# Kernel optimization log

Measured on AMD Instinct MI355X. Metric: run time of the kernel, lower is better.

## Reference

```python
import jax, jax.numpy as jnp
import numpy as np

BIG = 1e9  # finite stand-in for float('inf') border padding (grad-safe)


def setup_inputs() -> dict:
    key = jax.random.key(0)
    k1, k2 = jax.random.split(key)
    B, L1, L2, F = 32, 1024, 1024, 128
    return {
        "seq1": jax.random.normal(k1, (B, L1, F), dtype=jnp.float32),
        "seq2": jax.random.normal(k2, (B, L2, F), dtype=jnp.float32),
        "scale_weights": jnp.ones((1,), dtype=jnp.float32),  # nn.Parameter ones(num_scales)/num_scales -> softmax-normalized anyway
    }


def _dtw_similarity(seq1, seq2):
    """Vectorized (anti-diagonal wavefront) version of MultiScaleDTW._compute_dtw.

    Same recurrence: D[i,j] = ||s1[i-1]-s2[j-1]|| + min(D[i-1,j-1], D[i-1,j], D[i,j-1]),
    D[0,0]=0, first row/col = inf. Returns similarity = 1/(1 + D[L1,L2]/(L1+L2)).
    """
    B, L1, F = seq1.shape
    L2 = seq2.shape[1]
    # pairwise L2 distance matrix (B, L1, L2) via |a|^2 + |b|^2 - 2 a.b (one GEMM)
    sq1 = jnp.sum(seq1 * seq1, axis=-1)
    sq2 = jnp.sum(seq2 * seq2, axis=-1)
    dot = jnp.einsum('bif,bjf->bij', seq1, seq2)
    C = jnp.sqrt(jnp.maximum(sq1[:, :, None] + sq2[:, None, :] - 2.0 * dot, 0.0))

    i_idx = jnp.arange(L1 + 1)
    # diagonal k holds D[i, k-i] for i in [0, L1]
    d0 = jnp.full((B, L1 + 1), BIG, jnp.float32).at[:, 0].set(0.0)  # k=0: D[0,0]=0
    d1 = jnp.full((B, L1 + 1), BIG, jnp.float32)                     # k=1: borders = inf

    def shift(x):  # x[:, i] -> x[:, i-1], pad with BIG
        return jnp.concatenate([jnp.full((B, 1), BIG, x.dtype), x[:, :-1]], axis=1)

    def step(carry, k):
        prev2, prev = carry  # diagonals k-2, k-1
        j = k - i_idx
        row = jnp.clip(i_idx - 1, 0, L1 - 1)
        col = jnp.clip(j - 1, 0, L2 - 1)
        c = C[:, row, col]  # (B, L1+1) cost along the diagonal
        m = jnp.minimum(shift(prev2), jnp.minimum(shift(prev), prev))
        cur = c + m
        valid = (i_idx >= 1) & (i_idx <= L1) & (j >= 1) & (j <= L2)
        cur = jnp.where(valid[None, :], cur, BIG)
        return (prev, cur), None

    (_, last), _ = jax.lax.scan(step, (d0, d1), jnp.arange(2, L1 + L2 + 1))
    dtw_dist = last[:, L1] / (L1 + L2)  # D[L1, L2] / (L1 + L2)
    return 1.0 / (1.0 + dtw_dist)


def reference(seq1, seq2, scale_weights):
    # num_scales = 1: softmax over single scale weight -> 1.0; only scale-0 DTW runs
    w = jax.nn.softmax(scale_weights, axis=0)
    sim = _dtw_similarity(seq1, seq2)
    return w[0] * sim  # combined_similarity, shape (B,)
```

## Files before the change

kernel.cpp:

```cpp
#include <hip/hip_runtime.h>
#include <hip/hip_bf16.h>

#define BIGV 1.0e9f

static constexpr int B_ = 32;
static constexpr int L_ = 1024;
static constexpr int F_ = 128;
static constexpr int S_ = 2;
static constexpr int UDIM_ = 1296;
static constexpr int LAG_ = 160;
static constexpr int NSEGG_ = 82;
static constexpr size_t STREAM_US = (size_t)B_ * 2 * UDIM_ * 512;

typedef __attribute__((ext_vector_type(8))) short short8;
typedef __attribute__((ext_vector_type(4))) float f32x4;

__device__ __forceinline__ unsigned pack2(float x, float y) {
  unsigned r;
  asm("v_cvt_pk_bf16_f32 %0, %1, %2" : "=v"(r) : "v"(x), "v"(y));
  return r;
}

__global__ void norm_kernel(const float* __restrict__ s1, const float* __restrict__ s2,
                            float* __restrict__ nrm) {
  int gt   = blockIdx.x * blockDim.x + threadIdx.x;
  int wid  = gt >> 6;
  int lane = gt & 63;
  const float* src = (wid < B_ * L_) ? (s1 + (size_t)wid * F_)
                                     : (s2 + (size_t)(wid - B_ * L_) * F_);
  float2 v = ((const float2*)src)[lane];
  float s = v.x * v.x + v.y * v.y;
#pragma unroll
  for (int o = 32; o > 0; o >>= 1) s += __shfl_xor(s, o, 64);
  if (lane == 0) nrm[wid] = s;
}

__global__ __launch_bounds__(256) void cost_kernel(const float* __restrict__ s1,
                                                   const float* __restrict__ s2,
                                                   ushort* __restrict__ stream,
                                                   const float* __restrict__ nrm) {
  __shared__ __align__(16) ushort sbuf[2 * 128 * 136];
  __shared__ float q1[128], q2[128];
  short (*aL)[136] = (short(*)[136])sbuf;
  short (*bL)[136] = (short(*)[136])(sbuf + 128 * 136);
  ushort (*stage)[136] = (ushort(*)[136])sbuf;

  const int tid = threadIdx.x;
  const int b   = blockIdx.y;
  const int tc  = blockIdx.x & 7;
  const int tr  = blockIdx.x >> 3;

  const float* Ap = s1 + (size_t)b * L_ * F_ + (size_t)tr * 128 * F_;
  const float* Bp = s2 + (size_t)b * L_ * F_ + (size_t)tc * 128 * F_;

#pragma unroll 4
  for (int it = 0; it < 16; ++it) {
    int idx = it * 1024 + tid * 4;
    int r = idx >> 7, cc = idx & 127;
    float4 va = *(const float4*)(Ap + idx);
    float4 vb = *(const float4*)(Bp + idx);
    *(uint2*)&aL[r][cc] = make_uint2(pack2(va.x, va.y), pack2(va.z, va.w));
    *(uint2*)&bL[r][cc] = make_uint2(pack2(vb.x, vb.y), pack2(vb.z, vb.w));
  }
  if (tid < 128) q1[tid] = nrm[(size_t)b * L_ + tr * 128 + tid];
  else           q2[tid - 128] = nrm[(size_t)B_ * L_ + (size_t)b * L_ + tc * 128 + (tid - 128)];
  __syncthreads();

  const int wave = tid >> 6, lane = tid & 63, quad = lane >> 4, l16 = lane & 15;
  const int m0 = (wave >> 1) * 64, n0 = (wave & 1) * 64;

  f32x4 acc[4][4] = {};
#pragma unroll
  for (int kc = 0; kc < 4; ++kc) {
    short8 af[4], bf[4];
#pragma unroll
    for (int mi = 0; mi < 4; ++mi)
      af[mi] = *(const short8*)&aL[m0 + mi * 16 + l16][kc * 32 + quad * 8];
#pragma unroll
    for (int nj = 0; nj < 4; ++nj)
      bf[nj] = *(const short8*)&bL[n0 + nj * 16 + l16][kc * 32 + quad * 8];
#pragma unroll
    for (int mi = 0; mi < 4; ++mi)
#pragma unroll
      for (int nj = 0; nj < 4; ++nj)
        acc[mi][nj] = __builtin_amdgcn_mfma_f32_16x16x32_bf16(af[mi], bf[nj], acc[mi][nj], 0, 0, 0);
  }

  __syncthreads();

#pragma unroll
  for (int mi = 0; mi < 4; ++mi) {
    int lr = m0 + mi * 16 + quad * 4;
    int du = 2 * (lr >> 3);
    float a0 = q1[lr + 0], a1 = q1[lr + 1], a2 = q1[lr + 2], a3 = q1[lr + 3];
#pragma unroll
    for (int nj = 0; nj < 4; ++nj) {
      int lc = n0 + nj * 16 + l16;
      float qc = q2[lc];
      float vx = sqrtf(fmaxf(a0 + qc - 2.0f * acc[mi][nj][0], 0.0f));
      float vy = sqrtf(fmaxf(a1 + qc - 2.0f * acc[mi][nj][1], 0.0f));
      float vz = sqrtf(fmaxf(a2 + qc - 2.0f * acc[mi][nj][2], 0.0f));
      float vw = sqrtf(fmaxf(a3 + qc - 2.0f * acc[mi][nj][3], 0.0f));
      *(uint2*)&stage[lc + du][lr] = make_uint2(pack2(vx, vy), pack2(vz, vw));
    }
  }
  __syncthreads();

  const int w      = tr >> 2;
  const int rlbase = (tr & 3) * 128;
  const int ubase  = tc * 128 + 32 * (tr & 3);
  ushort* Sb = stream + ((size_t)(b * 2 + w) * UDIM_ + ubase) * 512 + rlbase;
#pragma unroll
  for (int it = 0; it < 10; ++it) {
    int t = it * 256 + tid;
    if (t < 158 * 16) {
      int u = t >> 4, g = t & 15;
      if ((unsigned)(u - 2 * g) < 128u)
        *(uint4*)(Sb + (size_t)u * 512 + g * 8) = *(const uint4*)&stage[u][g * 8];
    }
  }
}

#define UNPACK_CV(cw, cv)                         \
  cv[0] = __uint_as_float((cw).x << 16);          \
  cv[1] = __uint_as_float((cw).x & 0xFFFF0000u);  \
  cv[2] = __uint_as_float((cw).y << 16);          \
  cv[3] = __uint_as_float((cw).y & 0xFFFF0000u);  \
  cv[4] = __uint_as_float((cw).z << 16);          \
  cv[5] = __uint_as_float((cw).z & 0xFFFF0000u);  \
  cv[6] = __uint_as_float((cw).w << 16);          \
  cv[7] = __uint_as_float((cw).w & 0xFFFF0000u);

#define CHAIN_BODY(head)                                            \
  {                                                                 \
    float cur = (head);                                             \
    float nl[8];                                                    \
    nl[0] = cur;                                                    \
    _Pragma("unroll") for (int r = 1; r < 8; ++r) {                 \
      cur = cv[r] + fminf(fminf(left[r - 1], left[r]), cur);        \
      nl[r] = cur;                                                  \
    }                                                               \
    _Pragma("unroll") for (int r = 0; r < 8; ++r) left[r] = nl[r];  \
    bot = nl[7];                                                    \
  }

__global__ __launch_bounds__(128, 1) void dtw_kernel(const ushort* __restrict__ stream,
                                                     float* __restrict__ out) {
  __shared__ float hand[1040];

  const int b    = blockIdx.x;
  const int tid  = threadIdx.x;
  const int wave = tid >> 6;
  const int lane = tid & 63;
  const bool l0 = (lane == 0);

  const ushort* src = stream + (size_t)(b * 2 + wave) * UDIM_ * 512 + lane * 8;

  float left[8];
#pragma unroll
  for (int r = 0; r < 8; ++r) left[r] = BIGV;
  float bot = BIGV;
  float sh[4] = {BIGV, BIGV, BIGV, BIGV};
  float hPrev = BIGV, result = 0.0f;
  float hRing[4];
  float hb[16];
  uint4 pre[16];

#pragma unroll
  for (int i = 0; i < 16; ++i) pre[i] = *(const uint4*)(src + (size_t)i * 512);

  for (int n = 0; n < NSEGG_; ++n) {
    __syncthreads();
    const int sBase = 16 * n - (wave ? LAG_ : 0);
    if ((unsigned)sBase >= 1152u) continue;

    const bool fast = (sBase >= 128) & (sBase <= 1008);

    if (wave == 0) {
      if (fast) {
#pragma unroll
        for (int k = 0; k < 16; ++k) {
          float shN = __shfl_up(bot, 1, 64);
          uint4 cw = pre[k];
          pre[k] = *(const uint4*)(src + (size_t)(sBase + k + 16) * 512);
          float cv[8];
          UNPACK_CV(cw, cv)
          float dgT = l0 ? BIGV : sh[(k + 2) & 3];
          float upT = l0 ? BIGV : sh[(k + 3) & 3];
          CHAIN_BODY(cv[0] + fminf(fminf(dgT, upT), left[0]))
          sh[k & 3] = shN;
          hb[k] = bot;
        }
        if (lane == 63) {
          float4* hp = (float4*)&hand[sBase - 126];
          hp[0] = make_float4(hb[0], hb[1], hb[2], hb[3]);
          hp[1] = make_float4(hb[4], hb[5], hb[6], hb[7]);
          hp[2] = make_float4(hb[8], hb[9], hb[10], hb[11]);
          hp[3] = make_float4(hb[12], hb[13], hb[14], hb[15]);
        }
      } else {
#pragma unroll
        for (int k = 0; k < 16; ++k) {
          const int s = sBase + k;
          const int col = s - S_ * lane;
          float shN = __shfl_up(bot, 1, 64);
          uint4 cw = pre[k];
          pre[k] = *(const uint4*)(src + (size_t)(sBase + k + 16) * 512);
          float cv[8];
          UNPACK_CV(cw, cv)
          float dgT = l0 ? ((s == 0) ? 0.0f : BIGV) : sh[(k + 2) & 3];
          float upT = l0 ? BIGV : sh[(k + 3) & 3];
          bool act = ((unsigned)col < 1024u);
          float c0 = act ? cv[0] : BIGV;
          CHAIN_BODY(c0 + fminf(fminf(dgT, upT), left[0]))
          sh[k & 3] = shN;
          int j = s - 126;
          if (lane == 63 && (unsigned)j < 1024u) hand[j] = bot;
        }
      }
    } else {
      if (fast) {
#pragma unroll
        for (int i = 0; i < 4; ++i) hRing[i] = hand[sBase + i];
#pragma unroll
        for (int k = 0; k < 16; ++k) {
          float shN = __shfl_up(bot, 1, 64);
          float hCur = hRing[k & 3];
          uint4 cw = pre[k];
          pre[k] = *(const uint4*)(src + (size_t)(sBase + k + 16) * 512);
          hRing[k & 3] = hand[sBase + k + 4];
          float cv[8];
          UNPACK_CV(cw, cv)
          float dgT = l0 ? hPrev : sh[(k + 2) & 3];
          float upT = l0 ? hCur : sh[(k + 3) & 3];
          CHAIN_BODY(cv[0] + fminf(fminf(dgT, upT), left[0]))
          sh[k & 3] = shN;
          hPrev = hCur;
        }
      } else {
#pragma unroll
        for (int i = 0; i < 4; ++i) hRing[i] = hand[(sBase + i) & 1023];
#pragma unroll
        for (int k = 0; k < 16; ++k) {
          const int s = sBase + k;
          const int col = s - S_ * lane;
          float shN = __shfl_up(bot, 1, 64);
          float hCur = hRing[k & 3];
          uint4 cw = pre[k];
          pre[k] = *(const uint4*)(src + (size_t)(sBase + k + 16) * 512);
          hRing[k & 3] = hand[(s + 4) & 1023];
          float cv[8];
          UNPACK_CV(cw, cv)
          float dgT = l0 ? ((s == 0) ? BIGV : hPrev) : sh[(k + 2) & 3];
          float upT = l0 ? hCur : sh[(k + 3) & 3];
          bool act = ((unsigned)col < 1024u);
          float c0 = act ? cv[0] : BIGV;
          CHAIN_BODY(c0 + fminf(fminf(dgT, upT), left[0]))
          sh[k & 3] = shN;
          hPrev = hCur;
          if (s == 1149) result = bot;
        }
      }
    }
  }
  if (wave == 1 && lane == 63) out[b] = 1.0f / (1.0f + result * (1.0f / 2048.0f));
}

extern "C" void kernel_launch(void* const* d_in, const int* in_sizes, int n_in,
                              void* d_out, int out_size, void* d_ws, size_t ws_size,
                              hipStream_t stream_) {
  const float* s1 = (const float*)d_in[0];
  const float* s2 = (const float*)d_in[1];
  float* out = (float*)d_out;
  ushort* cws = (ushort*)d_ws;
  float* nrm = (float*)(cws + STREAM_US);

  norm_kernel<<<dim3((2 * B_ * L_) / 4), 256, 0, stream_>>>(s1, s2, nrm);
  cost_kernel<<<dim3(64, B_), 256, 0, stream_>>>(s1, s2, cws, nrm);
  dtw_kernel<<<dim3(B_), 128, 0, stream_>>>(cws, out);
}
```

Measured before the change: 237.6 us.

## Split DTW wavefront across four waves with four rows per lane

Each batch's DTW recurrence now runs on four pipelined waves instead of two, each lane handling four rows rather than eight. This shortens the serial dependency chain per diagonal step. The cost-stream layout is repacked to 256-row slices per wave, and boundary rows are handed between consecutive waves through per-wave LDS buffers. In exchange there are more lagged segments, more block barriers and more per-step shuffle overhead relative to the arithmetic.

Result: slower. 256.6 us (+8.0%).

```diff
diff --git a/kernel.cpp b/kernel.cpp
--- a/kernel.cpp
+++ b/kernel.cpp
@@ -9,8 +9,8 @@
 static constexpr int S_ = 2;
 static constexpr int UDIM_ = 1296;
 static constexpr int LAG_ = 160;
-static constexpr int NSEGG_ = 82;
-static constexpr size_t STREAM_US = (size_t)B_ * 2 * UDIM_ * 512;
+static constexpr int NSEGG_ = 102;
+static constexpr size_t STREAM_US = (size_t)B_ * 4 * UDIM_ * 256;
 
 typedef __attribute__((ext_vector_type(8))) short short8;
 typedef __attribute__((ext_vector_type(4))) float f32x4;
@@ -91,7 +91,7 @@
 #pragma unroll
   for (int mi = 0; mi < 4; ++mi) {
     int lr = m0 + mi * 16 + quad * 4;
-    int du = 2 * (lr >> 3);
+    int du = 2 * (lr >> 2);
     float a0 = q1[lr + 0], a1 = q1[lr + 1], a2 = q1[lr + 2], a3 = q1[lr + 3];
 #pragma unroll
     for (int nj = 0; nj < 4; ++nj) {
@@ -106,93 +106,89 @@
   }
   __syncthreads();
 
-  const int w      = tr >> 2;
-  const int rlbase = (tr & 3) * 128;
-  const int ubase  = tc * 128 + 32 * (tr & 3);
-  ushort* Sb = stream + ((size_t)(b * 2 + w) * UDIM_ + ubase) * 512 + rlbase;
-#pragma unroll
-  for (int it = 0; it < 10; ++it) {
+  const int w      = tr >> 1;
+  const int rlbase = (tr & 1) * 128;
+  const int ubase  = tc * 128 + 64 * (tr & 1);
+  ushort* Sb = stream + ((size_t)(b * 4 + w) * UDIM_ + ubase) * 256 + rlbase;
+#pragma unroll
+  for (int it = 0; it < 24; ++it) {
     int t = it * 256 + tid;
-    if (t < 158 * 16) {
-      int u = t >> 4, g = t & 15;
+    if (t < 190 * 32) {
+      int u = t >> 5, g = t & 31;
       if ((unsigned)(u - 2 * g) < 128u)
-        *(uint4*)(Sb + (size_t)u * 512 + g * 8) = *(const uint4*)&stage[u][g * 8];
+        *(uint2*)(Sb + (size_t)u * 256 + g * 4) = *(const uint2*)&stage[u][g * 4];
     }
   }
 }
 
-#define UNPACK_CV(cw, cv)                         \
+#define UNPACK_CV4(cw, cv)                        \
   cv[0] = __uint_as_float((cw).x << 16);          \
   cv[1] = __uint_as_float((cw).x & 0xFFFF0000u);  \
   cv[2] = __uint_as_float((cw).y << 16);          \
-  cv[3] = __uint_as_float((cw).y & 0xFFFF0000u);  \
-  cv[4] = __uint_as_float((cw).z << 16);          \
-  cv[5] = __uint_as_float((cw).z & 0xFFFF0000u);  \
-  cv[6] = __uint_as_float((cw).w << 16);          \
-  cv[7] = __uint_as_float((cw).w & 0xFFFF0000u);
-
-#define CHAIN_BODY(head)                                            \
+  cv[3] = __uint_as_float((cw).y & 0xFFFF0000u);
+
+#define CHAIN_BODY4(head)                                           \
   {                                                                 \
     float cur = (head);                                             \
-    float nl[8];                                                    \
+    float nl[4];                                                    \
     nl[0] = cur;                                                    \
-    _Pragma("unroll") for (int r = 1; r < 8; ++r) {                 \
+    _Pragma("unroll") for (int r = 1; r < 4; ++r) {                 \
       cur = cv[r] + fminf(fminf(left[r - 1], left[r]), cur);        \
       nl[r] = cur;                                                  \
     }                                                               \
-    _Pragma("unroll") for (int r = 0; r < 8; ++r) left[r] = nl[r];  \
-    bot = nl[7];                                                    \
-  }
-
-__global__ __launch_bounds__(128, 1) void dtw_kernel(const ushort* __restrict__ stream,
+    _Pragma("unroll") for (int r = 0; r < 4; ++r) left[r] = nl[r];  \
+    bot = nl[3];                                                    \
+  }
+
+__global__ __launch_bounds__(256, 1) void dtw_kernel(const ushort* __restrict__ stream,
                                                      float* __restrict__ out) {
-  __shared__ float hand[1040];
+  __shared__ float hand[3][1040];
 
   const int b    = blockIdx.x;
   const int tid  = threadIdx.x;
-  const int wave = tid >> 6;
+  const int w    = tid >> 6;
   const int lane = tid & 63;
   const bool l0 = (lane == 0);
 
-  const ushort* src = stream + (size_t)(b * 2 + wave) * UDIM_ * 512 + lane * 8;
-
-  float left[8];
-#pragma unroll
-  for (int r = 0; r < 8; ++r) left[r] = BIGV;
+  const ushort* src = stream + (size_t)(b * 4 + w) * UDIM_ * 256 + lane * 4;
+
+  float left[4];
+#pragma unroll
+  for (int r = 0; r < 4; ++r) left[r] = BIGV;
   float bot = BIGV;
   float sh[4] = {BIGV, BIGV, BIGV, BIGV};
   float hPrev = BIGV, result = 0.0f;
   float hRing[4];
   float hb[16];
-  uint4 pre[16];
-
-#pragma unroll
-  for (int i = 0; i < 16; ++i) pre[i] = *(const uint4*)(src + (size_t)i * 512);
+  uint2 pre[16];
+
+#pragma unroll
+  for (int i = 0; i < 16; ++i) pre[i] = *(const uint2*)(src + (size_t)i * 256);
 
   for (int n = 0; n < NSEGG_; ++n) {
     __syncthreads();
-    const int sBase = 16 * n - (wave ? LAG_ : 0);
+    const int sBase = 16 * n - w * LAG_;
     if ((unsigned)sBase >= 1152u) continue;
 
     const bool fast = (sBase >= 128) & (sBase <= 1008);
 
-    if (wave == 0) {
+    if (w == 0) {
       if (fast) {
 #pragma unroll
         for (int k = 0; k < 16; ++k) {
           float shN = __shfl_up(bot, 1, 64);
-          uint4 cw = pre[k];
-          pre[k] = *(const uint4*)(src + (size_t)(sBase + k + 16) * 512);
-          float cv[8];
-          UNPACK_CV(cw, cv)
+          uint2 cw = pre[k];
+          pre[k] = *(const uint2*)(src + (size_t)(sBase + k + 16) * 256);
+          float cv[4];
+          UNPACK_CV4(cw, cv)
           float dgT = l0 ? BIGV : sh[(k + 2) & 3];
           float upT = l0 ? BIGV : sh[(k + 3) & 3];
-          CHAIN_BODY(cv[0] + fminf(fminf(dgT, upT), left[0]))
+          CHAIN_BODY4(cv[0] + fminf(fminf(dgT, upT), left[0]))
           sh[k & 3] = shN;
           hb[k] = bot;
         }
         if (lane == 63) {
-          float4* hp = (float4*)&hand[sBase - 126];
+          float4* hp = (float4*)&hand[0][sBase - 126];
           hp[0] = make_float4(hb[0], hb[1], hb[2], hb[3]);
           hp[1] = make_float4(hb[4], hb[5], hb[6], hb[7]);
           hp[2] = make_float4(hb[8], hb[9], hb[10], hb[11]);
@@ -204,66 +200,121 @@
           const int s = sBase + k;
           const int col = s - S_ * lane;
           float shN = __shfl_up(bot, 1, 64);
-          uint4 cw = pre[k];
-          pre[k] = *(const uint4*)(src + (size_t)(sBase + k + 16) * 512);
-          float cv[8];
-          UNPACK_CV(cw, cv)
+          uint2 cw = pre[k];
+          pre[k] = *(const uint2*)(src + (size_t)(sBase + k + 16) * 256);
+          float cv[4];
+          UNPACK_CV4(cw, cv)
           float dgT = l0 ? ((s == 0) ? 0.0f : BIGV) : sh[(k + 2) & 3];
           float upT = l0 ? BIGV : sh[(k + 3) & 3];
           bool act = ((unsigned)col < 1024u);
           float c0 = act ? cv[0] : BIGV;
-          CHAIN_BODY(c0 + fminf(fminf(dgT, upT), left[0]))
+          CHAIN_BODY4(c0 + fminf(fminf(dgT, upT), left[0]))
           sh[k & 3] = shN;
           int j = s - 126;
-          if (lane == 63 && (unsigned)j < 1024u) hand[j] = bot;
+          if (lane == 63 && (unsigned)j < 1024u) hand[0][j] = bot;
         }
       }
-    } else {
+    } else if (w == 3) {
+      const float* hs = hand[2];
       if (fast) {
 #pragma unroll
-        for (int i = 0; i < 4; ++i) hRing[i] = hand[sBase + i];
+        for (int i = 0; i < 4; ++i) hRing[i] = hs[sBase + i];
 #pragma unroll
         for (int k = 0; k < 16; ++k) {
           float shN = __shfl_up(bot, 1, 64);
           float hCur = hRing[k & 3];
-          uint4 cw = pre[k];
-          pre[k] = *(const uint4*)(src + (size_t)(sBase + k + 16) * 512);
-          hRing[k & 3] = hand[sBase + k + 4];
-          float cv[8];
-          UNPACK_CV(cw, cv)
+          uint2 cw = pre[k];
+          pre[k] = *(const uint2*)(src + (size_t)(sBase + k + 16) * 256);
+          hRing[k & 3] = hs[sBase + k + 4];
+          float cv[4];
+          UNPACK_CV4(cw, cv)
           float dgT = l0 ? hPrev : sh[(k + 2) & 3];
           float upT = l0 ? hCur : sh[(k + 3) & 3];
-          CHAIN_BODY(cv[0] + fminf(fminf(dgT, upT), left[0]))
+          CHAIN_BODY4(cv[0] + fminf(fminf(dgT, upT), left[0]))
           sh[k & 3] = shN;
           hPrev = hCur;
         }
       } else {
 #pragma unroll
-        for (int i = 0; i < 4; ++i) hRing[i] = hand[(sBase + i) & 1023];
+        for (int i = 0; i < 4; ++i) hRing[i] = hs[(sBase + i) & 1023];
 #pragma unroll
         for (int k = 0; k < 16; ++k) {
           const int s = sBase + k;
           const int col = s - S_ * lane;
           float shN = __shfl_up(bot, 1, 64);
           float hCur = hRing[k & 3];
-          uint4 cw = pre[k];
-          pre[k] = *(const uint4*)(src + (size_t)(sBase + k + 16) * 512);
-          hRing[k & 3] = hand[(s + 4) & 1023];
-          float cv[8];
-          UNPACK_CV(cw, cv)
+          uint2 cw = pre[k];
+          pre[k] = *(const uint2*)(src + (size_t)(sBase + k + 16) * 256);
+          hRing[k & 3] = hs[(s + 4) & 1023];
+          float cv[4];
+          UNPACK_CV4(cw, cv)
           float dgT = l0 ? ((s == 0) ? BIGV : hPrev) : sh[(k + 2) & 3];
           float upT = l0 ? hCur : sh[(k + 3) & 3];
           bool act = ((unsigned)col < 1024u);
           float c0 = act ? cv[0] : BIGV;
-          CHAIN_BODY(c0 + fminf(fminf(dgT, upT), left[0]))
+          CHAIN_BODY4(c0 + fminf(fminf(dgT, upT), left[0]))
           sh[k & 3] = shN;
           hPrev = hCur;
           if (s == 1149) result = bot;
         }
       }
+    } else {
+      const float* hs = hand[w - 1];
+      float* hd = hand[w];
+      if (fast) {
+#pragma unroll
+        for (int i = 0; i < 4; ++i) hRing[i] = hs[sBase + i];
+#pragma unroll
+        for (int k = 0; k < 16; ++k) {
+          float shN = __shfl_up(bot, 1, 64);
+          float hCur = hRing[k & 3];
+          uint2 cw = pre[k];
+          pre[k] = *(const uint2*)(src + (size_t)(sBase + k + 16) * 256);
+          hRing[k & 3] = hs[sBase + k + 4];
+          float cv[4];
+          UNPACK_CV4(cw, cv)
+          float dgT = l0 ? hPrev : sh[(k + 2) & 3];
+          float upT = l0 ? hCur : sh[(k + 3) & 3];
+          CHAIN_BODY4(cv[0] + fminf(fminf(dgT, upT), left[0]))
+          sh[k & 3] = shN;
+          hPrev = hCur;
+          hb[k] = bot;
+        }
+        if (lane == 63) {
+          float4* hp = (float4*)&hd[sBase - 126];
+          hp[0] = make_float4(hb[0], hb[1], hb[2], hb[3]);
+          hp[1] = make_float4(hb[4], hb[5], hb[6], hb[7]);
+          hp[2] = make_float4(hb[8], hb[9], hb[10], hb[11]);
+          hp[3] = make_float4(hb[12], hb[13], hb[14], hb[15]);
+        }
+      } else {
+#pragma unroll
+        for (int i = 0; i < 4; ++i) hRing[i] = hs[(sBase + i) & 1023];
+#pragma unroll
+        for (int k = 0; k < 16; ++k) {
+          const int s = sBase + k;
+          const int col = s - S_ * lane;
+          float shN = __shfl_up(bot, 1, 64);
+          float hCur = hRing[k & 3];
+          uint2 cw = pre[k];
+          pre[k] = *(const uint2*)(src + (size_t)(sBase + k + 16) * 256);
+          hRing[k & 3] = hs[(s + 4) & 1023];
+          float cv[4];
+          UNPACK_CV4(cw, cv)
+          float dgT = l0 ? ((s == 0) ? BIGV : hPrev) : sh[(k + 2) & 3];
+          float upT = l0 ? hCur : sh[(k + 3) & 3];
+          bool act = ((unsigned)col < 1024u);
+          float c0 = act ? cv[0] : BIGV;
+          CHAIN_BODY4(c0 + fminf(fminf(dgT, upT), left[0]))
+          sh[k & 3] = shN;
+          hPrev = hCur;
+          int j = s - 126;
+          if (lane == 63 && (unsigned)j < 1024u) hd[j] = bot;
+        }
+      }
     }
   }
-  if (wave == 1 && lane == 63) out[b] = 1.0f / (1.0f + result * (1.0f / 2048.0f));
+  if (w == 3 && lane == 63) out[b] = 1.0f / (1.0f + result * (1.0f / 2048.0f));
 }
 
 extern "C" void kernel_launch(void* const* d_in, const int* in_sizes, int n_in,
@@ -277,5 +328,5 @@
 
   norm_kernel<<<dim3((2 * B_ * L_) / 4), 256, 0, stream_>>>(s1, s2, nrm);
   cost_kernel<<<dim3(64, B_), 256, 0, stream_>>>(s1, s2, cws, nrm);
-  dtw_kernel<<<dim3(B_), 128, 0, stream_>>>(cws, out);
-}
+  dtw_kernel<<<dim3(B_), 256, 0, stream_>>>(cws, out);
+}
```
